# Performance work log

Hardware: AMD Instinct MI355X
Metric: run time of the kernel (lower is better)

Reference implementation:

```python
import jax, jax.numpy as jnp
import numpy as np

W_DIM = 512
CHANNELS = 1024
SIZE = 64            # H = W = 64
SAMPLING_RATE = 64.0
BANDWIDTH = 2.0


def setup_inputs() -> dict:
    key = jax.random.key(0)
    k_w, k_f, k_p, k_wt, k_aw = jax.random.split(key, 5)
    B = 16
    w = jax.random.normal(k_w, (B, W_DIM), dtype=jnp.float32)
    # freqs init as in SynthesisInput.__init__
    freqs = jax.random.normal(k_f, (CHANNELS, 2), dtype=jnp.float32)
    radii = jnp.sqrt(jnp.sum(freqs ** 2, axis=1, keepdims=True))
    freqs = freqs / (radii * jnp.exp(radii ** 2) ** 0.25) * BANDWIDTH
    phases = jax.random.uniform(k_p, (CHANNELS,), dtype=jnp.float32) - 0.5
    weight = jax.random.normal(k_wt, (CHANNELS, CHANNELS), dtype=jnp.float32)
    # affine FC layer (weight_init=0 in original; use small random for a useful test)
    affine_w = jax.random.normal(k_aw, (4, W_DIM), dtype=jnp.float32) * 0.1
    affine_b = jnp.array([1.0, 0.0, 0.0, 0.0], dtype=jnp.float32)
    return {"w": w, "freqs": freqs, "phases": phases, "weight": weight,
            "affine_w": affine_w, "affine_b": affine_b}


def _forward(w, freqs, phases, weight, affine_w, affine_b):
    B = w.shape[0]
    C = freqs.shape[0]
    H = Wd = SIZE
    # affine: FullyConnectedLayer gain = 1/sqrt(in_features)
    t = w @ affine_w.T / jnp.sqrt(jnp.float32(W_DIM)) + affine_b  # [B,4]
    t = t / jnp.linalg.norm(t[:, :2], axis=1, keepdims=True)
    c, s = t[:, 0], t[:, 1]
    # rotation block of m_r (identity base transform, so transform_ = m_r @ m_t)
    R = jnp.stack([jnp.stack([c, -s], -1), jnp.stack([s, c], -1)], -2)  # [B,2,2]
    # translation column: transform_[:, :2, 2] = R @ (-t[:,2:4])
    trans_col = -jnp.einsum('bij,bj->bi', R, t[:, 2:4])                 # [B,2]
    phases_b = phases[None, :] + jnp.einsum('cd,bd->bc', freqs, trans_col)  # [B,C]
    freqs_b = jnp.einsum('cd,bde->bce', freqs, R)                           # [B,C,2]
    amps = jnp.clip(
        1.0 - (jnp.linalg.norm(freqs_b, axis=2) - BANDWIDTH)
        / (SAMPLING_RATE / 2 - BANDWIDTH), 0.0, 1.0)                        # [B,C]
    # affine_grid (align_corners=False): normalized coords (2i+1)/N - 1, scaled
    sx = 0.5 * Wd / SAMPLING_RATE
    sy = 0.5 * H / SAMPLING_RATE
    u = ((jnp.arange(Wd, dtype=jnp.float32) + 0.5) / Wd * 2.0 - 1.0) * sx  # x (width)
    v = ((jnp.arange(H, dtype=jnp.float32) + 0.5) / H * 2.0 - 1.0) * sy    # y (height)
    grid = jnp.stack(jnp.meshgrid(u, v, indexing='xy'), axis=-1)           # [H,W,2]
    x = jnp.einsum('hwd,bcd->bhwc', grid, freqs_b) + phases_b[:, None, None, :]
    x = jnp.sin(x * (2.0 * jnp.pi)) * amps[:, None, None, :]
    x = jnp.einsum('bhwc,kc->bhwk', x, weight / jnp.sqrt(jnp.float32(C)))
    return jnp.transpose(x, (0, 3, 1, 2))  # [B,C,H,W]


def reference(w, freqs, phases, weight, affine_w, affine_b):
    return _forward(w, freqs, phases, weight, affine_w, affine_b)
```

## Files before the change

kernel.cpp:

```cpp
#include <hip/hip_runtime.h>

typedef __attribute__((ext_vector_type(4))) float f32x4;
typedef __attribute__((ext_vector_type(8))) short s16x8;

#define W_DIM   512
#define CHANNELS 1024
#define SPATIAL 4096
#define NB      16

__device__ inline unsigned short f2bf(float x){
  unsigned int u = __float_as_uint(x);
  u += 0x7fffu + ((u >> 16) & 1u);
  return (unsigned short)(u >> 16);
}

__device__ inline float sin2pi(float x){
  return __builtin_amdgcn_sinf(__builtin_amdgcn_fractf(x));
}

__device__ inline void async_load16(const unsigned short* g, unsigned short* l){
  __builtin_amdgcn_global_load_lds(
      (const __attribute__((address_space(1))) void*)g,
      (__attribute__((address_space(3))) void*)l, 16, 0, 0);
}

__global__ void sy_setup(const float* __restrict__ w, const float* __restrict__ freqs,
                         const float* __restrict__ phases, const float* __restrict__ affine_w,
                         const float* __restrict__ affine_b, float4* __restrict__ params){
  int b = blockIdx.x;
  int t = threadIdx.x;
  float p0=0.f, p1=0.f, p2=0.f, p3=0.f;
  #pragma unroll
  for (int it = 0; it < 2; ++it){
    int i = t + it*256;
    float wv = w[b*W_DIM + i];
    p0 += wv * affine_w[0*W_DIM + i];
    p1 += wv * affine_w[1*W_DIM + i];
    p2 += wv * affine_w[2*W_DIM + i];
    p3 += wv * affine_w[3*W_DIM + i];
  }
  #pragma unroll
  for (int off = 32; off >= 1; off >>= 1){
    p0 += __shfl_down(p0, off);
    p1 += __shfl_down(p1, off);
    p2 += __shfl_down(p2, off);
    p3 += __shfl_down(p3, off);
  }
  __shared__ float red[4][4];
  __shared__ float sc[4];
  int wave = t >> 6, lane = t & 63;
  if (lane == 0){ red[wave][0]=p0; red[wave][1]=p1; red[wave][2]=p2; red[wave][3]=p3; }
  __syncthreads();
  if (t == 0){
    const float inv_sq = 0.04419417382415922f;
    float tv[4];
    #pragma unroll
    for (int j=0;j<4;++j){
      float s = red[0][j]+red[1][j]+red[2][j]+red[3][j];
      tv[j] = s * inv_sq + affine_b[j];
    }
    float n  = sqrtf(tv[0]*tv[0] + tv[1]*tv[1]);
    float iv = 1.0f / n;
    float c = tv[0]*iv, s = tv[1]*iv;
    float t2 = tv[2]*iv, t3 = tv[3]*iv;
    float tcx = -(c*t2 - s*t3);
    float tcy = -(s*t2 + c*t3);
    sc[0]=c; sc[1]=s; sc[2]=tcx; sc[3]=tcy;
  }
  __syncthreads();
  float c = sc[0], s = sc[1], tcx = sc[2], tcy = sc[3];
  #pragma unroll
  for (int j = 0; j < 4; ++j){
    int ci = t + j*256;
    float f0x = freqs[ci*2], f0y = freqs[ci*2+1];
    float fx =  f0x*c + f0y*s;
    float fy = -f0x*s + f0y*c;
    float ph = phases[ci] + f0x*tcx + f0y*tcy;
    float r  = sqrtf(fx*fx + fy*fy);
    float amp = 1.0f - (r - 2.0f) * (1.0f/30.0f);
    amp = fminf(fmaxf(amp, 0.0f), 1.0f);
    float4 P; P.x=fx; P.y=fy; P.z=ph; P.w=amp;
    params[b*CHANNELS + ci] = P;
  }
}

__global__ void sy_cvtw(const float* __restrict__ wt, unsigned short* __restrict__ Wbf){
  int i = (blockIdx.x*256 + threadIdx.x)*4;
  float4 v = *(const float4*)(wt + i);
  ushort4 o;
  o.x = f2bf(v.x*0.03125f); o.y = f2bf(v.y*0.03125f);
  o.z = f2bf(v.z*0.03125f); o.w = f2bf(v.w*0.03125f);
  *(ushort4*)(Wbf + i) = o;
}

__global__ void sy_genS(const float4* __restrict__ params, unsigned short* __restrict__ Sbf,
                        int b0){
  int blk = blockIdx.x;
  int bb  = blk >> 7;
  int b   = b0 + bb;
  int m0  = (blk & 127) * 32;
  int t   = threadIdx.x;
  int c0  = t * 4;
  float4 P0 = params[b*CHANNELS + c0 + 0];
  float4 P1 = params[b*CHANNELS + c0 + 1];
  float4 P2 = params[b*CHANNELS + c0 + 2];
  float4 P3 = params[b*CHANNELS + c0 + 3];
  int h = m0 >> 6;
  float v = (h + 0.5f) * (1.0f/64.0f) - 0.5f;
  float a0 = v*P0.y + P0.z, a1 = v*P1.y + P1.z;
  float a2 = v*P2.y + P2.z, a3 = v*P3.y + P3.z;
  unsigned short* dst = Sbf + ((size_t)bb * SPATIAL + m0) * CHANNELS + c0;
  for (int im = 0; im < 32; ++im){
    int wv = (m0 + im) & 63;
    float u = (wv + 0.5f) * (1.0f/64.0f) - 0.5f;
    ushort4 o;
    o.x = f2bf(sin2pi(u*P0.x + a0) * P0.w);
    o.y = f2bf(sin2pi(u*P1.x + a1) * P1.w);
    o.z = f2bf(sin2pi(u*P2.x + a2) * P2.w);
    o.w = f2bf(sin2pi(u*P3.x + a3) * P3.w);
    *(ushort4*)(dst + (size_t)im * CHANNELS) = o;
  }
}

__global__ __launch_bounds__(256) void sy_gemm(const unsigned short* __restrict__ Wbf,
                                               const unsigned short* __restrict__ Sbf,
                                               float* __restrict__ out, int b0){
  __shared__ unsigned short lA[128*32];
  __shared__ unsigned short lB[128*32];
  const int nt = blockIdx.x, mt = blockIdx.y, bb = blockIdx.z;
  const int b = b0 + bb;
  const int tid  = threadIdx.x;
  const int lane = tid & 63, wave = tid >> 6;
  const int wm = wave & 1, wn = wave >> 1;
  const int Mbase = mt * 128, Nbase = nt * 128;

  const int q0 = wave*128 + lane, q1 = q0 + 64;
  const unsigned short* gA0 = Wbf + (size_t)(Mbase + (q0>>2))*CHANNELS + (q0&3)*8;
  const unsigned short* gA1 = Wbf + (size_t)(Mbase + (q1>>2))*CHANNELS + (q1&3)*8;
  const unsigned short* gB0 = Sbf + ((size_t)bb*SPATIAL + Nbase + (q0>>2))*CHANNELS + (q0&3)*8;
  const unsigned short* gB1 = Sbf + ((size_t)bb*SPATIAL + Nbase + (q1>>2))*CHANNELS + (q1&3)*8;
  unsigned short* lA0 = lA + q0*8;
  unsigned short* lA1 = lA + q1*8;
  unsigned short* lB0 = lB + q0*8;
  unsigned short* lB1 = lB + q1*8;

  f32x4 acc[4][4];
  #pragma unroll
  for (int i=0;i<4;++i)
    #pragma unroll
    for (int j=0;j<4;++j){
      f32x4 z = {0.f,0.f,0.f,0.f};
      acc[i][j] = z;
    }

  const int koff = (lane >> 4) * 8;
  const int rA = (wm*64 + (lane & 15))*32 + koff;
  const int rB = (wn*64 + (lane & 15))*32 + koff;

  for (int kt = 0; kt < 32; ++kt){
    const int ko = kt * 32;
    async_load16(gA0 + ko, lA0);
    async_load16(gA1 + ko, lA1);
    async_load16(gB0 + ko, lB0);
    async_load16(gB1 + ko, lB1);
    __syncthreads();
    s16x8 af[4], bv[4];
    #pragma unroll
    for (int i=0;i<4;++i) af[i] = *(const s16x8*)&lA[rA + i*512];
    #pragma unroll
    for (int j=0;j<4;++j) bv[j] = *(const s16x8*)&lB[rB + j*512];
    #pragma unroll
    for (int i=0;i<4;++i)
      #pragma unroll
      for (int j=0;j<4;++j)
        acc[i][j] = __builtin_amdgcn_mfma_f32_16x16x32_bf16(af[i], bv[j], acc[i][j], 0, 0, 0);
    __syncthreads();
  }

  float* outb = out + (size_t)b * CHANNELS * SPATIAL;
  const int col  = Nbase + wn*64 + (lane & 15);
  const int row0 = Mbase + wm*64 + ((lane >> 4) << 2);
  #pragma unroll
  for (int i=0;i<4;++i)
    #pragma unroll
    for (int j=0;j<4;++j)
      #pragma unroll
      for (int r=0;r<4;++r)
        outb[(size_t)(row0 + i*16 + r) * SPATIAL + (col + j*16)] = acc[i][j][r];
}

__global__ void sy_fallback(const float* __restrict__ weight, const float4* __restrict__ params,
                            float* __restrict__ out){
  extern __shared__ float S[];
  int b  = blockIdx.x >> 7;
  int m0 = (blockIdx.x & 127) * 32;
  int t  = threadIdx.x;
  {
    int c0 = t*4;
    float4 P0 = params[b*CHANNELS+c0+0], P1 = params[b*CHANNELS+c0+1];
    float4 P2 = params[b*CHANNELS+c0+2], P3 = params[b*CHANNELS+c0+3];
    int h = m0 >> 6;
    float v = (h + 0.5f)*(1.0f/64.0f) - 0.5f;
    float a0 = v*P0.y+P0.z, a1 = v*P1.y+P1.z, a2 = v*P2.y+P2.z, a3 = v*P3.y+P3.z;
    for (int im = 0; im < 32; ++im){
      int wv = (m0+im) & 63;
      float u = (wv+0.5f)*(1.0f/64.0f) - 0.5f;
      float* row = S + im*CHANNELS + c0;
      row[0] = sin2pi(u*P0.x+a0)*P0.w;
      row[1] = sin2pi(u*P1.x+a1)*P1.w;
      row[2] = sin2pi(u*P2.x+a2)*P2.w;
      row[3] = sin2pi(u*P3.x+a3)*P3.w;
    }
  }
  __syncthreads();
  for (int oi = t; oi < 32*1024; oi += 256){
    int k = oi >> 5, im = oi & 31;
    const float4* wr = (const float4*)(weight + (size_t)k*CHANNELS);
    const float4* sr = (const float4*)(S + im*CHANNELS);
    float sum = 0.f;
    for (int c4 = 0; c4 < CHANNELS/4; ++c4){
      float4 a = wr[c4], s4 = sr[c4];
      sum += a.x*s4.x + a.y*s4.y + a.z*s4.z + a.w*s4.w;
    }
    out[((size_t)b*CHANNELS + k)*SPATIAL + m0 + im] = sum * 0.03125f;
  }
}

extern "C" void kernel_launch(void* const* d_in, const int* in_sizes, int n_in,
                              void* d_out, int out_size, void* d_ws, size_t ws_size,
                              hipStream_t stream){
  const float* w        = (const float*)d_in[0];
  const float* freqs    = (const float*)d_in[1];
  const float* phases   = (const float*)d_in[2];
  const float* weight   = (const float*)d_in[3];
  const float* affine_w = (const float*)d_in[4];
  const float* affine_b = (const float*)d_in[5];
  float* out = (float*)d_out;

  char* ws = (char*)d_ws;
  float4* params = (float4*)ws;
  const size_t off_w = 262144;
  const size_t off_s = off_w + 2097152;
  unsigned short* Wbf = (unsigned short*)(ws + off_w);
  unsigned short* Sbf = (unsigned short*)(ws + off_s);
  const size_t per_batch = (size_t)SPATIAL * CHANNELS * 2;

  sy_setup<<<NB, 256, 0, stream>>>(w, freqs, phases, affine_w, affine_b, params);

  int G = 0;
  if (ws_size >= off_s + per_batch){
    size_t avail = (ws_size - off_s) / per_batch;
    G = avail >= (size_t)NB ? NB : (int)avail;
  }
  if (G == 0){
    sy_fallback<<<NB*128, 256, 32*1024*4, stream>>>(weight, params, out);
    return;
  }
  sy_cvtw<<<1024, 256, 0, stream>>>(weight, Wbf);
  for (int b0 = 0; b0 < NB; b0 += G){
    int g = (NB - b0) < G ? (NB - b0) : G;
    sy_genS<<<g*128, 256, 0, stream>>>(params, Sbf, b0);
    dim3 grid(32, 8, g);
    sy_gemm<<<grid, 256, 0, stream>>>(Wbf, Sbf, out, b0);
  }
}
```

Measured before the change: 502.6 us.

## Use angle-addition recurrence in sine generation and remap LDS layout for GEMM

The S-matrix generator now computes per-channel sin/cos of the row and column terms once, then steps along width with a rotation recurrence instead of one hardware sin per element. It writes 8 channels per thread with 16-byte stores. The GEMM tile loader also remaps which rows and k-chunks each lane fetches, so LDS holds fragments in MFMA-friendly order and reads are conflict-free. The recurrence adds error that compounds over 16 steps, and the transcendental cost it saves may be small next to memory traffic.

```diff
diff --git a/kernel.cpp b/kernel.cpp
--- a/kernel.cpp
+++ b/kernel.cpp
@@ -2,6 +2,7 @@
 
 typedef __attribute__((ext_vector_type(4))) float f32x4;
 typedef __attribute__((ext_vector_type(8))) short s16x8;
+typedef __attribute__((ext_vector_type(8))) unsigned short u16x8;
 
 #define W_DIM   512
 #define CHANNELS 1024
@@ -16,6 +17,9 @@
 
 __device__ inline float sin2pi(float x){
   return __builtin_amdgcn_sinf(__builtin_amdgcn_fractf(x));
+}
+__device__ inline float cos2pi(float x){
+  return __builtin_amdgcn_cosf(__builtin_amdgcn_fractf(x));
 }
 
 __device__ inline void async_load16(const unsigned short* g, unsigned short* l){
@@ -100,25 +104,40 @@
   int b   = b0 + bb;
   int m0  = (blk & 127) * 32;
   int t   = threadIdx.x;
-  int c0  = t * 4;
-  float4 P0 = params[b*CHANNELS + c0 + 0];
-  float4 P1 = params[b*CHANNELS + c0 + 1];
-  float4 P2 = params[b*CHANNELS + c0 + 2];
-  float4 P3 = params[b*CHANNELS + c0 + 3];
-  int h = m0 >> 6;
-  float v = (h + 0.5f) * (1.0f/64.0f) - 0.5f;
-  float a0 = v*P0.y + P0.z, a1 = v*P1.y + P1.z;
-  float a2 = v*P2.y + P2.z, a3 = v*P3.y + P3.z;
-  unsigned short* dst = Sbf + ((size_t)bb * SPATIAL + m0) * CHANNELS + c0;
-  for (int im = 0; im < 32; ++im){
-    int wv = (m0 + im) & 63;
-    float u = (wv + 0.5f) * (1.0f/64.0f) - 0.5f;
-    ushort4 o;
-    o.x = f2bf(sin2pi(u*P0.x + a0) * P0.w);
-    o.y = f2bf(sin2pi(u*P1.x + a1) * P1.w);
-    o.z = f2bf(sin2pi(u*P2.x + a2) * P2.w);
-    o.w = f2bf(sin2pi(u*P3.x + a3) * P3.w);
-    *(ushort4*)(dst + (size_t)im * CHANNELS) = o;
+  int c0  = (t & 127) * 8;
+  int mh  = t >> 7;
+  int h   = m0 >> 6;
+  int w0  = (m0 + mh*16) & 63;
+  float v  = (h  + 0.5f) * (1.0f/64.0f) - 0.5f;
+  float u0 = (w0 + 0.5f) * (1.0f/64.0f) - 0.5f;
+
+  float sU[8], cU[8], sV[8], cV[8], sD[8], cD[8];
+  #pragma unroll
+  for (int j = 0; j < 8; ++j){
+    float4 P = params[b*CHANNELS + c0 + j];
+    float V = v*P.y + P.z;
+    sV[j] = sin2pi(V) * P.w;
+    cV[j] = cos2pi(V) * P.w;
+    float U = u0*P.x;
+    sU[j] = sin2pi(U);
+    cU[j] = cos2pi(U);
+    float D = P.x * (1.0f/64.0f);
+    sD[j] = sin2pi(D);
+    cD[j] = cos2pi(D);
+  }
+
+  unsigned short* dst = Sbf + ((size_t)bb * SPATIAL + m0 + mh*16) * CHANNELS + c0;
+  for (int im = 0; im < 16; ++im){
+    u16x8 o;
+    #pragma unroll
+    for (int j = 0; j < 8; ++j){
+      float val = sU[j]*cV[j] + cU[j]*sV[j];
+      o[j] = f2bf(val);
+      float ns = sU[j]*cD[j] + cU[j]*sD[j];
+      float nc = cU[j]*cD[j] - sU[j]*sD[j];
+      sU[j] = ns; cU[j] = nc;
+    }
+    *(u16x8*)(dst + (size_t)im * CHANNELS) = o;
   }
 }
 
@@ -135,10 +154,12 @@
   const int Mbase = mt * 128, Nbase = nt * 128;
 
   const int q0 = wave*128 + lane, q1 = q0 + 64;
-  const unsigned short* gA0 = Wbf + (size_t)(Mbase + (q0>>2))*CHANNELS + (q0&3)*8;
-  const unsigned short* gA1 = Wbf + (size_t)(Mbase + (q1>>2))*CHANNELS + (q1&3)*8;
-  const unsigned short* gB0 = Sbf + ((size_t)bb*SPATIAL + Nbase + (q0>>2))*CHANNELS + (q0&3)*8;
-  const unsigned short* gB1 = Sbf + ((size_t)bb*SPATIAL + Nbase + (q1>>2))*CHANNELS + (q1&3)*8;
+  const int r0 = (q0>>6)*16 + (q0&15), k0 = ((q0>>4)&3)*8;
+  const int r1 = (q1>>6)*16 + (q1&15), k1 = ((q1>>4)&3)*8;
+  const unsigned short* gA0 = Wbf + (size_t)(Mbase + r0)*CHANNELS + k0;
+  const unsigned short* gA1 = Wbf + (size_t)(Mbase + r1)*CHANNELS + k1;
+  const unsigned short* gB0 = Sbf + ((size_t)bb*SPATIAL + Nbase + r0)*CHANNELS + k0;
+  const unsigned short* gB1 = Sbf + ((size_t)bb*SPATIAL + Nbase + r1)*CHANNELS + k1;
   unsigned short* lA0 = lA + q0*8;
   unsigned short* lA1 = lA + q1*8;
   unsigned short* lB0 = lB + q0*8;
@@ -153,9 +174,8 @@
       acc[i][j] = z;
     }
 
-  const int koff = (lane >> 4) * 8;
-  const int rA = (wm*64 + (lane & 15))*32 + koff;
-  const int rB = (wn*64 + (lane & 15))*32 + koff;
+  const int rA = wm*2048 + (lane>>4)*128 + (lane&15)*8;
+  const int rB = wn*2048 + (lane>>4)*128 + (lane&15)*8;
 
   for (int kt = 0; kt < 32; ++kt){
     const int ko = kt * 32;
```

Result: slower. 562.8 us (+12.0%).
